# Kernel optimization log

Hardware: AMD Instinct MI355X
Metric: run time of the kernel (lower is better)

The kernel has to match this reference:

```python
import jax, jax.numpy as jnp
import numpy as np

B, ORDER, S, D, H = 64, 2, 256, 256, 8
HD = D // H  # head_dim = 32


def setup_inputs() -> dict:
    key = jax.random.key(0)
    ks = jax.random.split(key, 6)
    stdv = 1.0 / np.sqrt(HD)
    return {
        "x": jax.random.normal(ks[0], (B, ORDER, S, D), jnp.float32),
        "A": jax.random.randint(ks[1], (B, ORDER, S, S), 0, 5, jnp.int32),
        # params stacked as [order, conv(1|2), ...]
        "Wp": jax.random.normal(ks[2], (ORDER, 2, D, D), jnp.float32) * stdv,
        "bp": jnp.zeros((ORDER, 2, D), jnp.float32),
        "att_src": jax.random.normal(ks[3], (ORDER, 2, H, HD), jnp.float32) * stdv,
        "att_dst": jax.random.normal(ks[4], (ORDER, 2, H, HD), jnp.float32) * stdv,
        "gbias": jnp.zeros((ORDER, 2, D), jnp.float32),
        "prelu_a": 0.25 * jnp.ones((D,), jnp.float32),
    }


def _gat(x, edge, W, b, a_src, a_dst, gb):
    """Dense additive GAT over a [B,S,S] boolean adjacency. Eval mode (dropout inert)."""
    Bt, St, Dt = x.shape
    x = x @ W + b                                   # project (bias=True)
    xh = x.reshape(Bt, St, H, HD)
    a_s = jnp.einsum('bshd,hd->bsh', xh, a_src)     # per-source score
    a_d = jnp.einsum('bthd,hd->bth', xh, a_dst)     # per-dest score
    alpha = a_s[:, :, None, :] + a_d[:, None, :, :]  # [B, S_src, S_dst, H]
    alpha = jnp.where(edge[..., None], alpha, 0.0)   # masked_fill((A != 1), 0)
    alpha = jnp.where(alpha >= 0, alpha, 0.2 * alpha)  # leaky_relu(0.2)
    alpha = jax.nn.softmax(alpha, axis=1)            # stable softmax over source axis
    out = jnp.einsum('bsth,bshd->bthd', alpha, xh).reshape(Bt, St, Dt)
    return out + x + gb                              # add_self_loops + bias


def reference(x, A, Wp, bp, att_src, att_dst, gbias, prelu_a):
    # A1 = (A==2)+(A==4); A2 = (A==3)+(A==4); edge iff value == 1
    A1 = (A == 2) | (A == 4)
    A2 = (A == 3) | (A == 4)
    hs = []
    for i in range(ORDER):  # order is a small structural constant (=2)
        h1 = _gat(x[:, i], A1[:, i], Wp[i, 0], bp[i, 0], att_src[i, 0], att_dst[i, 0], gbias[i, 0])
        h2 = _gat(x[:, i], A2[:, i], Wp[i, 1], bp[i, 1], att_src[i, 1], att_dst[i, 1], gbias[i, 1])
        hs.append(h1 + h2)
    h = jnp.stack(hs, axis=1)                       # [B, order, S, D]
    out = h + h.mean(axis=1, keepdims=True)
    out = jnp.where(out >= 0, out, prelu_a * out)   # PReLU(dim)
    return out
```

## Files before the change

### kernel.cpp

```cpp
#include <hip/hip_runtime.h>
#include <hip/hip_bf16.h>
#include <math.h>

typedef __bf16 bf16;
typedef __bf16 bf16x4 __attribute__((ext_vector_type(4)));
typedef __bf16 bf16x8 __attribute__((ext_vector_type(8)));
typedef float f32x4 __attribute__((ext_vector_type(4)));

#define LOG2E 1.44269504f

__device__ inline float fast_exp2(float x) {
#if __has_builtin(__builtin_amdgcn_exp2f)
    return __builtin_amdgcn_exp2f(x);
#else
    return exp2f(x);
#endif
}


__global__ void prep_wt(const float* __restrict__ Wp, bf16* __restrict__ Wt) {
    int gid = blockIdx.x * 256 + threadIdx.x;
    int k  = gid & 255;
    int n  = (gid >> 8) & 255;
    int ij = gid >> 16;
    Wt[gid] = (bf16)Wp[(ij * 256 + k) * 256 + n];
}

__launch_bounds__(256)
__global__ void proj_gemm(const float* __restrict__ x, const bf16* __restrict__ Wt,
                          const float* __restrict__ bp, bf16* __restrict__ xpb) {
    __shared__ bf16 As[128][40];
    __shared__ bf16 Bs[128][40];

    int tid = threadIdx.x;
    int mt = blockIdx.x, nt = blockIdx.y, i = blockIdx.z;
    int n0 = nt * 128;
    int j  = n0 >> 8;
    int d0 = n0 & 255;
    int m0 = mt * 128;

    int mr = tid >> 1;
    int kq = (tid & 1) * 16;
    int m  = m0 + mr;
    int b  = m >> 8, s = m & 255;
    const float* xrow = x + (((size_t)(b * 2 + i) * 256 + s) << 8);
    const bf16*  wrow = Wt + (((size_t)(i * 2 + j) * 256 + d0 + mr) << 8);

    int wave = tid >> 6, lane = tid & 63;
    int wm = (wave & 1) * 64, wn = (wave >> 1) * 64;
    int lrow = lane & 15, quad = lane >> 4;

    f32x4 acc[4][4];
#pragma unroll
    for (int a = 0; a < 4; ++a)
#pragma unroll
        for (int c = 0; c < 4; ++c) acc[a][c] = (f32x4){0.f, 0.f, 0.f, 0.f};

    for (int kc = 0; kc < 8; ++kc) {
        int k0 = kc * 32;
        const float* ap = xrow + k0 + kq;
        f32x4 xa0 = *(const f32x4*)(ap);
        f32x4 xa1 = *(const f32x4*)(ap + 4);
        f32x4 xa2 = *(const f32x4*)(ap + 8);
        f32x4 xa3 = *(const f32x4*)(ap + 12);
        bf16x8 w0, w1;
#pragma unroll
        for (int q = 0; q < 4; ++q) {
            w0[q] = (bf16)xa0[q]; w0[q + 4] = (bf16)xa1[q];
            w1[q] = (bf16)xa2[q]; w1[q + 4] = (bf16)xa3[q];
        }
        *(bf16x8*)&As[mr][kq]     = w0;
        *(bf16x8*)&As[mr][kq + 8] = w1;
        const bf16* bpr = wrow + k0 + kq;
        *(bf16x8*)&Bs[mr][kq]     = *(const bf16x8*)bpr;
        *(bf16x8*)&Bs[mr][kq + 8] = *(const bf16x8*)(bpr + 8);
        __syncthreads();
        bf16x8 af[4], bfr[4];
#pragma unroll
        for (int mi = 0; mi < 4; ++mi)
            af[mi] = *(const bf16x8*)&As[wm + mi * 16 + lrow][quad * 8];
#pragma unroll
        for (int ni = 0; ni < 4; ++ni)
            bfr[ni] = *(const bf16x8*)&Bs[wn + ni * 16 + lrow][quad * 8];
#pragma unroll
        for (int mi = 0; mi < 4; ++mi)
#pragma unroll
            for (int ni = 0; ni < 4; ++ni)
                acc[mi][ni] = __builtin_amdgcn_mfma_f32_16x16x32_bf16(af[mi], bfr[ni], acc[mi][ni], 0, 0, 0);
        __syncthreads();
    }

#pragma unroll
    for (int mi = 0; mi < 4; ++mi) {
#pragma unroll
        for (int r = 0; r < 4; ++r) {
            int rowm = m0 + wm + mi * 16 + quad * 4 + r;
            int bb = rowm >> 8, ss = rowm & 255;
            size_t obase = (((size_t)(i * 2 + j) * 64 + bb) * 256 + ss) << 8;
#pragma unroll
            for (int ni = 0; ni < 4; ++ni) {
                int dcol = d0 + wn + ni * 16 + lrow;
                float v = acc[mi][ni][r] + bp[(i * 2 + j) * 256 + dcol];
                xpb[obase + dcol] = (bf16)v;
            }
        }
    }
}

__global__ void score_k(const bf16* __restrict__ xpb, const float* __restrict__ att_src,
                        const float* __restrict__ att_dst, float* __restrict__ asb,
                        float* __restrict__ adb) {
    int gid = blockIdx.x * 256 + threadIdx.x;
    int h = gid & 7;
    int r = gid >> 3;
    int s = r & 255;
    int bij = r >> 8;
    int ij = bij >> 6;
    const bf16* row = xpb + ((size_t)r << 8) + h * 32;
    const float* asrc = att_src + (ij * 8 + h) * 32;
    const float* adst = att_dst + (ij * 8 + h) * 32;
    float ssum = 0.f, dsum = 0.f;
#pragma unroll
    for (int c = 0; c < 4; ++c) {
        bf16x8 v = *(const bf16x8*)(row + c * 8);
#pragma unroll
        for (int q = 0; q < 8; ++q) {
            float f = (float)v[q];
            ssum += f * asrc[c * 8 + q];
            dsum += f * adst[c * 8 + q];
        }
    }
    int oidx = (bij * 8 + h) * 256 + s;
    asb[oidx] = ssum * LOG2E;
    adb[oidx] = dsum * LOG2E;
}

__global__ void pack_a(const int* __restrict__ A, unsigned* __restrict__ m1,
                       unsigned* __restrict__ m2) {
    int bid = blockIdx.x;
    int sh = bid & 1;
    int ijb = bid >> 1;
    int tid = threadIdx.x;
    const int* Ab = A + ((size_t)ijb << 16);
    unsigned w1 = 0, w2 = 0;
#pragma unroll 8
    for (int sl = 0; sl < 128; ++sl) {
        int s = sh * 128 + sl;
        int av = Ab[s * 256 + tid];
        unsigned f1 = (av == 2 || av == 4) ? 1u : 0u;
        unsigned f2 = (av == 3 || av == 4) ? 1u : 0u;
        w1 |= f1 << (s & 31);
        w2 |= f2 << (s & 31);
        if ((s & 31) == 31) {
            int kc = s >> 5;
            m1[(ijb * 8 + kc) * 256 + tid] = w1;
            m2[(ijb * 8 + kc) * 256 + tid] = w2;
            w1 = 0; w2 = 0;
        }
    }
}

__launch_bounds__(256, 3)
__global__ void attn_k(const bf16* __restrict__ xpb, const unsigned* __restrict__ m1,
                       const unsigned* __restrict__ m2, const float* __restrict__ asb,
                       const float* __restrict__ adb, const float* __restrict__ gbias,
                       float* __restrict__ out) {
    int bid = blockIdx.x;
    int tt = bid & 3, hg = (bid >> 2) & 1, i = (bid >> 3) & 1, b = bid >> 4;
    int t0 = tt * 64;
    int tid = threadIdx.x, wave = tid >> 6, lane = tid & 63;
    int lrow = lane & 15, quad = lane >> 4;
    int h = hg * 4 + wave;

    __shared__ float    as_l[2][4][256];
    __shared__ unsigned ml[2][8][64];
    __shared__ float    l_lds[2][4][64];

#pragma unroll
    for (int p = 0; p < 8; ++p) {
        int c = p >> 2, w = p & 3;
        as_l[c][w][tid] = asb[(((i * 2 + c) * 64 + b) * 8 + hg * 4 + w) * 256 + tid];
    }
    {
        const unsigned* mp0 = m1 + ((b * 2 + i) * 8) * 256 + t0;
        const unsigned* mp1 = m2 + ((b * 2 + i) * 8) * 256 + t0;
#pragma unroll
        for (int p = 0; p < 4; ++p) {
            int idx = p * 256 + tid;
            int c = idx >> 9, kc = (idx >> 6) & 7, tl = idx & 63;
            ml[c][kc][tl] = (c == 0 ? mp0 : mp1)[kc * 256 + tl];
        }
    }
    float ad_r[2][4];
#pragma unroll
    for (int c = 0; c < 2; ++c)
#pragma unroll
        for (int mi = 0; mi < 4; ++mi)
            ad_r[c][mi] = adb[(((i * 2 + c) * 64 + b) * 8 + h) * 256 + t0 + mi * 16 + lrow];
    __syncthreads();

    const bf16* xp0 = xpb + ((size_t)((i * 2 + 0) * 64 + b) << 16);
    const bf16* xp1 = xpb + ((size_t)((i * 2 + 1) * 64 + b) << 16);

    f32x4 acc[2][4][2];
#pragma unroll
    for (int c = 0; c < 2; ++c)
#pragma unroll
        for (int mi = 0; mi < 4; ++mi)
#pragma unroll
            for (int ni = 0; ni < 2; ++ni) acc[c][mi][ni] = (f32x4){0.f, 0.f, 0.f, 0.f};
    float lsum[2][4] = {{0.f, 0.f, 0.f, 0.f}, {0.f, 0.f, 0.f, 0.f}};

    for (int kc = 0; kc < 8; ++kc) {
        int s0 = kc * 32;
        bf16x8 bfr[2][2];
#pragma unroll
        for (int ni = 0; ni < 2; ++ni) {
            const bf16* vb0 = xp0 + (size_t)(s0 + quad * 8) * 256 + h * 32 + ni * 16 + lrow;
            const bf16* vb1 = xp1 + (size_t)(s0 + quad * 8) * 256 + h * 32 + ni * 16 + lrow;
#pragma unroll
            for (int j = 0; j < 8; ++j) {
                bfr[0][ni][j] = vb0[j * 256];
                bfr[1][ni][j] = vb1[j * 256];
            }
        }
#pragma unroll
        for (int c = 0; c < 2; ++c) {
            float asv[8];
#pragma unroll
            for (int j = 0; j < 8; ++j) asv[j] = as_l[c][wave][s0 + quad * 8 + j];
#pragma unroll
            for (int mi = 0; mi < 4; ++mi) {
                unsigned w = ml[c][kc][mi * 16 + lrow];
                float ad = ad_r[c][mi];
                bf16x8 af;
#pragma unroll
                for (int j = 0; j < 8; ++j) {
                    float u = asv[j] + ad;
                    u = fmaxf(u, 0.2f * u);
                    u = fminf(u, 115.f);
                    float e = fast_exp2(u);
                    e = ((w >> (quad * 8 + j)) & 1u) ? e : 1.0f;
                    lsum[c][mi] += e;
                    af[j] = (bf16)e;
                }
                acc[c][mi][0] = __builtin_amdgcn_mfma_f32_16x16x32_bf16(af, bfr[c][0], acc[c][mi][0], 0, 0, 0);
                acc[c][mi][1] = __builtin_amdgcn_mfma_f32_16x16x32_bf16(af, bfr[c][1], acc[c][mi][1], 0, 0, 0);
            }
        }
    }

#pragma unroll
    for (int c = 0; c < 2; ++c)
#pragma unroll
        for (int mi = 0; mi < 4; ++mi) {
            float l = lsum[c][mi];
            l += __shfl_xor(l, 16, 64);
            l += __shfl_xor(l, 32, 64);
            if (lane < 16) l_lds[c][wave][mi * 16 + lane] = l;
        }
    __syncthreads();

#pragma unroll
    for (int ni = 0; ni < 2; ++ni) {
        int dcol = h * 32 + ni * 16 + lrow;
        float gb = gbias[(i * 2 + 0) * 256 + dcol] + gbias[(i * 2 + 1) * 256 + dcol];
#pragma unroll
        for (int mi = 0; mi < 4; ++mi) {
#pragma unroll
            for (int r = 0; r < 4; ++r) {
                int tl = mi * 16 + quad * 4 + r;
                int t = t0 + tl;
                float inv1 = __builtin_amdgcn_rcpf(l_lds[0][wave][tl]);
                float inv2 = __builtin_amdgcn_rcpf(l_lds[1][wave][tl]);
                float res = (float)xp0[(size_t)t * 256 + dcol] + (float)xp1[(size_t)t * 256 + dcol];
                float v = acc[0][mi][ni][r] * inv1 + acc[1][mi][ni][r] * inv2 + res + gb;
                out[(((size_t)((b * 2 + i) * 256 + t)) << 8) + dcol] = v;
            }
        }
    }
}

__global__ void final_k(float* __restrict__ out, const float* __restrict__ prelu_a) {
    int gid = blockIdx.x * 256 + threadIdx.x;
    int d4 = gid & 63;
    int s  = (gid >> 6) & 255;
    int b  = gid >> 14;
    f32x4* o = (f32x4*)out;
    size_t i0 = (((size_t)(b * 2 + 0) * 256 + s) << 6) + d4;
    size_t i1 = (((size_t)(b * 2 + 1) * 256 + s) << 6) + d4;
    f32x4 h0 = o[i0], h1 = o[i1];
    f32x4 pa = *(const f32x4*)(prelu_a + d4 * 4);
    f32x4 v0, v1;
#pragma unroll
    for (int c = 0; c < 4; ++c) {
        float mn = 0.5f * (h0[c] + h1[c]);
        float a0 = h0[c] + mn;
        float a1 = h1[c] + mn;
        v0[c] = a0 >= 0.f ? a0 : pa[c] * a0;
        v1[c] = a1 >= 0.f ? a1 : pa[c] * a1;
    }
    o[i0] = v0;
    o[i1] = v1;
}

extern "C" void kernel_launch(void* const* d_in, const int* in_sizes, int n_in,
                              void* d_out, int out_size, void* d_ws, size_t ws_size,
                              hipStream_t stream) {
    const float* x       = (const float*)d_in[0];
    const int*   A       = (const int*)d_in[1];
    const float* Wp      = (const float*)d_in[2];
    const float* bp      = (const float*)d_in[3];
    const float* att_src = (const float*)d_in[4];
    const float* att_dst = (const float*)d_in[5];
    const float* gbias   = (const float*)d_in[6];
    const float* prelu_a = (const float*)d_in[7];
    float* out = (float*)d_out;

    char* ws = (char*)d_ws;
    bf16*     Wt  = (bf16*)ws;
    bf16*     xpb = (bf16*)(ws + 524288);
    float*    asb = (float*)(ws + 34078720);
    float*    adb = (float*)(ws + 36175872);
    unsigned* m1  = (unsigned*)(ws + 38273024);
    unsigned* m2  = (unsigned*)(ws + 39321600);

    prep_wt<<<1024, 256, 0, stream>>>(Wp, Wt);
    pack_a<<<256, 256, 0, stream>>>(A, m1, m2);
    dim3 gproj(128, 4, 2);
    proj_gemm<<<gproj, 256, 0, stream>>>(x, Wt, bp, xpb);
    score_k<<<2048, 256, 0, stream>>>(xpb, att_src, att_dst, asb, adb);
    attn_k<<<1024, 256, 0, stream>>>(xpb, m1, m2, asb, adb, gbias, out);
    final_k<<<4096, 256, 0, stream>>>(out, prelu_a);
}
```

Baseline: 238.5 us.

## Pre-convert x to bf16, use global_load_lds in GEMM, transpose V per head

Merges the weight transpose, adjacency packing and a new x-to-bf16 conversion into one prep kernel. The projection GEMM then loads bf16 tiles straight into LDS with global_load_lds, dropping the padded layout. score_k also writes a per-head transposed copy of the projected features, which it stores in the buffer that held bf16 x. This lets attn_k fetch V fragments and residuals with vector loads instead of strided scalar gathers. The cost is an extra full pass writing and reading bf16 x and the transposed V, plus possible LDS bank conflicts from the unpadded 32-wide tiles.

```diff
diff --git a/kernel.cpp b/kernel.cpp
--- a/kernel.cpp
+++ b/kernel.cpp
@@ -6,6 +6,7 @@
 typedef __bf16 bf16x4 __attribute__((ext_vector_type(4)));
 typedef __bf16 bf16x8 __attribute__((ext_vector_type(8)));
 typedef float f32x4 __attribute__((ext_vector_type(4)));
+typedef unsigned int u32;
 
 #define LOG2E 1.44269504f
 
@@ -17,20 +18,60 @@
 #endif
 }
 
-
-__global__ void prep_wt(const float* __restrict__ Wp, bf16* __restrict__ Wt) {
-    int gid = blockIdx.x * 256 + threadIdx.x;
-    int k  = gid & 255;
-    int n  = (gid >> 8) & 255;
-    int ij = gid >> 16;
-    Wt[gid] = (bf16)Wp[(ij * 256 + k) * 256 + n];
+#define GL2LDS(gp, lp) __builtin_amdgcn_global_load_lds( \
+    (const __attribute__((address_space(1))) u32*)(gp),  \
+    (__attribute__((address_space(3))) u32*)(lp), 16, 0, 0)
+
+
+__global__ void prep_k(const float* __restrict__ x, const float* __restrict__ Wp,
+                       const int* __restrict__ A, bf16* __restrict__ xb,
+                       bf16* __restrict__ Wt, unsigned* __restrict__ m1,
+                       unsigned* __restrict__ m2) {
+    int bid = blockIdx.x;
+    int tid = threadIdx.x;
+    if (bid < 4096) {
+        int gid = bid * 256 + tid;
+        const f32x4* xp = (const f32x4*)x + (size_t)gid * 2;
+        f32x4 a = xp[0], b4 = xp[1];
+        bf16x8 o;
+#pragma unroll
+        for (int c = 0; c < 4; ++c) { o[c] = (bf16)a[c]; o[c + 4] = (bf16)b4[c]; }
+        ((bf16x8*)xb)[gid] = o;
+    } else if (bid < 5120) {
+        int gid = (bid - 4096) * 256 + tid;
+        int k = gid & 255;
+        int n = (gid >> 8) & 255;
+        int ij = gid >> 16;
+        Wt[gid] = (bf16)Wp[(ij * 256 + k) * 256 + n];
+    } else {
+        int pb = bid - 5120;
+        int sh = pb & 1;
+        int ijb = pb >> 1;
+        const int* Ab = A + ((size_t)ijb << 16);
+        unsigned w1 = 0, w2 = 0;
+#pragma unroll 8
+        for (int sl = 0; sl < 128; ++sl) {
+            int s = sh * 128 + sl;
+            int av = Ab[s * 256 + tid];
+            unsigned f1 = (av == 2 || av == 4) ? 1u : 0u;
+            unsigned f2 = (av == 3 || av == 4) ? 1u : 0u;
+            w1 |= f1 << (s & 31);
+            w2 |= f2 << (s & 31);
+            if ((s & 31) == 31) {
+                int kc = s >> 5;
+                m1[(ijb * 8 + kc) * 256 + tid] = w1;
+                m2[(ijb * 8 + kc) * 256 + tid] = w2;
+                w1 = 0; w2 = 0;
+            }
+        }
+    }
 }
 
 __launch_bounds__(256)
-__global__ void proj_gemm(const float* __restrict__ x, const bf16* __restrict__ Wt,
+__global__ void proj_gemm(const bf16* __restrict__ xb, const bf16* __restrict__ Wt,
                           const float* __restrict__ bp, bf16* __restrict__ xpb) {
-    __shared__ bf16 As[128][40];
-    __shared__ bf16 Bs[128][40];
+    __shared__ bf16 As[128 * 32];
+    __shared__ bf16 Bs[128 * 32];
 
     int tid = threadIdx.x;
     int mt = blockIdx.x, nt = blockIdx.y, i = blockIdx.z;
@@ -39,12 +80,18 @@
     int d0 = n0 & 255;
     int m0 = mt * 128;
 
-    int mr = tid >> 1;
-    int kq = (tid & 1) * 16;
-    int m  = m0 + mr;
-    int b  = m >> 8, s = m & 255;
-    const float* xrow = x + (((size_t)(b * 2 + i) * 256 + s) << 8);
-    const bf16*  wrow = Wt + (((size_t)(i * 2 + j) * 256 + d0 + mr) << 8);
+    int c0 = tid, c1 = tid + 256;
+    int r0 = c0 >> 2, k80 = (c0 & 3) * 8;
+    int r1 = c1 >> 2, k81 = (c1 & 3) * 8;
+    int gm0 = m0 + r0, gm1 = m0 + r1;
+    const bf16* ga0 = xb + (((size_t)((gm0 >> 8) * 2 + i) * 256 + (gm0 & 255)) << 8) + k80;
+    const bf16* ga1 = xb + (((size_t)((gm1 >> 8) * 2 + i) * 256 + (gm1 & 255)) << 8) + k81;
+    const bf16* gb0 = Wt + (((size_t)(i * 2 + j) * 256 + d0 + r0) << 8) + k80;
+    const bf16* gb1 = Wt + (((size_t)(i * 2 + j) * 256 + d0 + r1) << 8) + k81;
+    bf16* la0 = As + c0 * 8;
+    bf16* la1 = As + c1 * 8;
+    bf16* lb0 = Bs + c0 * 8;
+    bf16* lb1 = Bs + c1 * 8;
 
     int wave = tid >> 6, lane = tid & 63;
     int wm = (wave & 1) * 64, wn = (wave >> 1) * 64;
@@ -58,30 +105,18 @@
 
     for (int kc = 0; kc < 8; ++kc) {
         int k0 = kc * 32;
-        const float* ap = xrow + k0 + kq;
-        f32x4 xa0 = *(const f32x4*)(ap);
-        f32x4 xa1 = *(const f32x4*)(ap + 4);
-        f32x4 xa2 = *(const f32x4*)(ap + 8);
-        f32x4 xa3 = *(const f32x4*)(ap + 12);
-        bf16x8 w0, w1;
-#pragma unroll
-        for (int q = 0; q < 4; ++q) {
-            w0[q] = (bf16)xa0[q]; w0[q + 4] = (bf16)xa1[q];
-            w1[q] = (bf16)xa2[q]; w1[q + 4] = (bf16)xa3[q];
-        }
-        *(bf16x8*)&As[mr][kq]     = w0;
-        *(bf16x8*)&As[mr][kq + 8] = w1;
-        const bf16* bpr = wrow + k0 + kq;
-        *(bf16x8*)&Bs[mr][kq]     = *(const bf16x8*)bpr;
-        *(bf16x8*)&Bs[mr][kq + 8] = *(const bf16x8*)(bpr + 8);
+        GL2LDS(ga0 + k0, la0);
+        GL2LDS(ga1 + k0, la1);
+        GL2LDS(gb0 + k0, lb0);
+        GL2LDS(gb1 + k0, lb1);
         __syncthreads();
         bf16x8 af[4], bfr[4];
 #pragma unroll
         for (int mi = 0; mi < 4; ++mi)
-            af[mi] = *(const bf16x8*)&As[wm + mi * 16 + lrow][quad * 8];
+            af[mi] = *(const bf16x8*)&As[(wm + mi * 16 + lrow) * 32 + quad * 8];
 #pragma unroll
         for (int ni = 0; ni < 4; ++ni)
-            bfr[ni] = *(const bf16x8*)&Bs[wn + ni * 16 + lrow][quad * 8];
+            bfr[ni] = *(const bf16x8*)&Bs[(wn + ni * 16 + lrow) * 32 + quad * 8];
 #pragma unroll
         for (int mi = 0; mi < 4; ++mi)
 #pragma unroll
@@ -109,7 +144,7 @@
 
 __global__ void score_k(const bf16* __restrict__ xpb, const float* __restrict__ att_src,
                         const float* __restrict__ att_dst, float* __restrict__ asb,
-                        float* __restrict__ adb) {
+                        float* __restrict__ adb, bf16* __restrict__ Vt) {
     int gid = blockIdx.x * 256 + threadIdx.x;
     int h = gid & 7;
     int r = gid >> 3;
@@ -119,6 +154,7 @@
     const bf16* row = xpb + ((size_t)r << 8) + h * 32;
     const float* asrc = att_src + (ij * 8 + h) * 32;
     const float* adst = att_dst + (ij * 8 + h) * 32;
+    bf16* vout = Vt + (((size_t)(bij * 8 + h)) << 13) + s;
     float ssum = 0.f, dsum = 0.f;
 #pragma unroll
     for (int c = 0; c < 4; ++c) {
@@ -129,39 +165,16 @@
             ssum += f * asrc[c * 8 + q];
             dsum += f * adst[c * 8 + q];
         }
+#pragma unroll
+        for (int q = 0; q < 8; ++q) vout[(c * 8 + q) << 8] = v[q];
     }
     int oidx = (bij * 8 + h) * 256 + s;
     asb[oidx] = ssum * LOG2E;
     adb[oidx] = dsum * LOG2E;
 }
 
-__global__ void pack_a(const int* __restrict__ A, unsigned* __restrict__ m1,
-                       unsigned* __restrict__ m2) {
-    int bid = blockIdx.x;
-    int sh = bid & 1;
-    int ijb = bid >> 1;
-    int tid = threadIdx.x;
-    const int* Ab = A + ((size_t)ijb << 16);
-    unsigned w1 = 0, w2 = 0;
-#pragma unroll 8
-    for (int sl = 0; sl < 128; ++sl) {
-        int s = sh * 128 + sl;
-        int av = Ab[s * 256 + tid];
-        unsigned f1 = (av == 2 || av == 4) ? 1u : 0u;
-        unsigned f2 = (av == 3 || av == 4) ? 1u : 0u;
-        w1 |= f1 << (s & 31);
-        w2 |= f2 << (s & 31);
-        if ((s & 31) == 31) {
-            int kc = s >> 5;
-            m1[(ijb * 8 + kc) * 256 + tid] = w1;
-            m2[(ijb * 8 + kc) * 256 + tid] = w2;
-            w1 = 0; w2 = 0;
-        }
-    }
-}
-
 __launch_bounds__(256, 3)
-__global__ void attn_k(const bf16* __restrict__ xpb, const unsigned* __restrict__ m1,
+__global__ void attn_k(const bf16* __restrict__ Vt, const unsigned* __restrict__ m1,
                        const unsigned* __restrict__ m2, const float* __restrict__ asb,
                        const float* __restrict__ adb, const float* __restrict__ gbias,
                        float* __restrict__ out) {
@@ -199,8 +212,8 @@
             ad_r[c][mi] = adb[(((i * 2 + c) * 64 + b) * 8 + h) * 256 + t0 + mi * 16 + lrow];
     __syncthreads();
 
-    const bf16* xp0 = xpb + ((size_t)((i * 2 + 0) * 64 + b) << 16);
-    const bf16* xp1 = xpb + ((size_t)((i * 2 + 1) * 64 + b) << 16);
+    const bf16* vt0 = Vt + (((size_t)(((i * 2 + 0) * 64 + b) * 8 + h)) << 13);
+    const bf16* vt1 = Vt + (((size_t)(((i * 2 + 1) * 64 + b) * 8 + h)) << 13);
 
     f32x4 acc[2][4][2];
 #pragma unroll
@@ -216,13 +229,8 @@
         bf16x8 bfr[2][2];
 #pragma unroll
         for (int ni = 0; ni < 2; ++ni) {
-            const bf16* vb0 = xp0 + (size_t)(s0 + quad * 8) * 256 + h * 32 + ni * 16 + lrow;
-            const bf16* vb1 = xp1 + (size_t)(s0 + quad * 8) * 256 + h * 32 + ni * 16 + lrow;
-#pragma unroll
-            for (int j = 0; j < 8; ++j) {
-                bfr[0][ni][j] = vb0[j * 256];
-                bfr[1][ni][j] = vb1[j * 256];
-            }
+            bfr[0][ni] = *(const bf16x8*)(vt0 + (size_t)(ni * 16 + lrow) * 256 + s0 + quad * 8);
+            bfr[1][ni] = *(const bf16x8*)(vt1 + (size_t)(ni * 16 + lrow) * 256 + s0 + quad * 8);
         }
 #pragma unroll
         for (int c = 0; c < 2; ++c) {
@@ -265,15 +273,19 @@
     for (int ni = 0; ni < 2; ++ni) {
         int dcol = h * 32 + ni * 16 + lrow;
         float gb = gbias[(i * 2 + 0) * 256 + dcol] + gbias[(i * 2 + 1) * 256 + dcol];
+        const bf16* r0 = vt0 + (size_t)(ni * 16 + lrow) * 256 + t0;
+        const bf16* r1 = vt1 + (size_t)(ni * 16 + lrow) * 256 + t0;
 #pragma unroll
         for (int mi = 0; mi < 4; ++mi) {
+            bf16x4 rv0 = *(const bf16x4*)(r0 + mi * 16 + quad * 4);
+            bf16x4 rv1 = *(const bf16x4*)(r1 + mi * 16 + quad * 4);
 #pragma unroll
             for (int r = 0; r < 4; ++r) {
                 int tl = mi * 16 + quad * 4 + r;
                 int t = t0 + tl;
                 float inv1 = __builtin_amdgcn_rcpf(l_lds[0][wave][tl]);
                 float inv2 = __builtin_amdgcn_rcpf(l_lds[1][wave][tl]);
-                float res = (float)xp0[(size_t)t * 256 + dcol] + (float)xp1[(size_t)t * 256 + dcol];
+                float res = (float)rv0[r] + (float)rv1[r];
                 float v = acc[0][mi][ni][r] * inv1 + acc[1][mi][ni][r] * inv2 + res + gb;
                 out[(((size_t)((b * 2 + i) * 256 + t)) << 8) + dcol] = v;
             }
@@ -324,12 +336,12 @@
     float*    adb = (float*)(ws + 36175872);
     unsigned* m1  = (unsigned*)(ws + 38273024);
     unsigned* m2  = (unsigned*)(ws + 39321600);
-
-    prep_wt<<<1024, 256, 0, stream>>>(Wp, Wt);
-    pack_a<<<256, 256, 0, stream>>>(A, m1, m2);
+    bf16*     xbvt = (bf16*)(ws + 40370176);
+
+    prep_k<<<5376, 256, 0, stream>>>(x, Wp, A, xbvt, Wt, m1, m2);
     dim3 gproj(128, 4, 2);
-    proj_gemm<<<gproj, 256, 0, stream>>>(x, Wt, bp, xpb);
-    score_k<<<2048, 256, 0, stream>>>(xpb, att_src, att_dst, asb, adb);
-    attn_k<<<1024, 256, 0, stream>>>(xpb, m1, m2, asb, adb, gbias, out);
+    proj_gemm<<<gproj, 256, 0, stream>>>(xbvt, Wt, bp, xpb);
+    score_k<<<2048, 256, 0, stream>>>(xpb, att_src, att_dst, asb, adb, xbvt);
+    attn_k<<<1024, 256, 0, stream>>>(xbvt, m1, m2, asb, adb, gbias, out);
     final_k<<<4096, 256, 0, stream>>>(out, prelu_a);
 }
```

New measurement: 234.4 us. No clear change (-1.7%).
